# Kernel optimization log

Measured on AMD Instinct MI355X. Metric: run time of the kernel, lower is better.

The kernel has to match this reference:

```python
import jax, jax.numpy as jnp
import numpy as np

EPS = 1e-5

def _conv1x1(x, w):
    # x: (B, Cin, N, K), w: (Cout, Cin) -> (B, Cout, N, K)
    return jnp.einsum('oc,bcnk->bonk', w, x)

def _bn2d(x, gamma, beta):
    # eval-mode BN with running_mean=0, running_var=1 (fresh init)
    scale = gamma / jnp.sqrt(1.0 + EPS)
    return x * scale[None, :, None, None] + beta[None, :, None, None]

def setup_inputs() -> dict:
    key = jax.random.key(0)
    ks = jax.random.split(key, 10)
    B, Cin, N, K = 8, 64, 1024, 32
    Cout, M = 64, 8
    Cin2 = 2 * Cin  # kernel_input='w_neighbor'
    features = jax.random.normal(ks[0], (B, Cin, N, K), dtype=jnp.float32)
    points_xyz = jax.random.normal(ks[1], (B, 3, N, K), dtype=jnp.float32)
    # ScoreNet convs: mlp_channels [7,16,16,16,M]; first 3 have BN (no bias), last has bias
    w1 = jax.random.normal(ks[2], (16, 7), dtype=jnp.float32) * (2.0 / 7) ** 0.5
    w2 = jax.random.normal(ks[3], (16, 16), dtype=jnp.float32) * (2.0 / 16) ** 0.5
    w3 = jax.random.normal(ks[4], (16, 16), dtype=jnp.float32) * (2.0 / 16) ** 0.5
    w4 = jax.random.normal(ks[5], (M, 16), dtype=jnp.float32) * (2.0 / 16) ** 0.5
    b4 = jnp.zeros((M,), dtype=jnp.float32)
    g1 = jnp.ones((16,), jnp.float32); be1 = jnp.zeros((16,), jnp.float32)
    g2 = jnp.ones((16,), jnp.float32); be2 = jnp.zeros((16,), jnp.float32)
    g3 = jnp.ones((16,), jnp.float32); be3 = jnp.zeros((16,), jnp.float32)
    # weight bank: kaiming_normal on (M, 2Cin, Cout) -> stored as (2Cin, M, Cout)
    wb = jax.random.normal(ks[6], (Cin2, M, Cout), dtype=jnp.float32) * (2.0 / Cin2) ** 0.5
    bn_g = jnp.ones((Cout,), jnp.float32); bn_b = jnp.zeros((Cout,), jnp.float32)
    return dict(features=features, points_xyz=points_xyz,
                w1=w1, g1=g1, be1=be1, w2=w2, g2=g2, be2=be2,
                w3=w3, g3=g3, be3=be3, w4=w4, b4=b4,
                weight_bank=wb, bn_g=bn_g, bn_b=bn_b)

def reference(features, points_xyz, w1, g1, be1, w2, g2, be2, w3, g3, be3,
              w4, b4, weight_bank, bn_g, bn_b):
    B, Cin, N, K = features.shape
    M = weight_bank.shape[1]
    # kernel_input = 'w_neighbor': concat(feat - center, feat) -> (B, 2Cin, N, K)
    center_f = features[..., :1]
    feat = jnp.concatenate([features - center_f, features], axis=1)
    # scorenet input = 'w_neighbor_dist': (center_xyz, xyz_diff, dist) -> (B, 7, N, K)
    center_xyz = jnp.broadcast_to(points_xyz[..., :1], points_xyz.shape)
    xyz_diff = points_xyz - center_xyz
    dist = jnp.sqrt(jnp.sum(xyz_diff * xyz_diff, axis=1, keepdims=True))
    xyz_feats = jnp.concatenate([center_xyz, xyz_diff, dist], axis=1)
    h = jax.nn.relu(_bn2d(_conv1x1(xyz_feats, w1), g1, be1))
    h = jax.nn.relu(_bn2d(_conv1x1(h, w2), g2, be2))
    h = jax.nn.relu(_bn2d(_conv1x1(h, w3), g3, be3))
    s = _conv1x1(h, w4) + b4[None, :, None, None]  # (B, M, N, K)
    scores = jax.nn.softmax(s, axis=1)
    scores = jnp.transpose(scores, (0, 2, 3, 1))  # (B, N, K, M)
    # matmul with weight bank then score-weighted sum over kernels, fused via einsum
    # original: (B,N,K,2Cin)@(2Cin,M*Cout) -> (B,N,K,M,Cout); sum_m scores * . -> (B,N,K,Cout)
    new_features = jnp.einsum('bcnk,cmo,bnkm->bonk', feat, weight_bank, scores)
    # BN2d (eval, fresh stats) + ReLU
    new_features = jax.nn.relu(_bn2d(new_features, bn_g, bn_b))
    return new_features
```

## Files before the change

kernel.cpp:

```cpp
#include <hip/hip_runtime.h>
#include <hip/hip_bf16.h>

typedef _Float16 f16;
typedef __attribute__((ext_vector_type(2))) _Float16 f16x2;
typedef __attribute__((ext_vector_type(8))) _Float16 f16x8;
typedef __attribute__((ext_vector_type(16))) float f32x16;

#define BNSCL 0.9999950000375f

__global__ __launch_bounds__(256) void k_scores(
    const float* __restrict__ xyz,
    const float* __restrict__ w1, const float* __restrict__ g1, const float* __restrict__ be1,
    const float* __restrict__ w2, const float* __restrict__ g2, const float* __restrict__ be2,
    const float* __restrict__ w3, const float* __restrict__ g3, const float* __restrict__ be3,
    const float* __restrict__ w4, const float* __restrict__ b4,
    const float* __restrict__ wb, f16* __restrict__ wbtA,
    f16* __restrict__ scores)
{
    __shared__ float lw[856];
    const int tid = threadIdx.x;

    if (blockIdx.x < 256) {
        int idx = blockIdx.x * 256 + tid;
        int j    = idx & 7;
        int lane = (idx >> 3) & 63;
        int ks   = (idx >> 9) & 31;
        int bank = (idx >> 14) & 1;
        int ot   = idx >> 15;
        int c    = ks * 2 + (lane >> 5);
        int o    = ot * 32 + (lane & 31);
        float vD = wb[(c * 8 + j) * 64 + o];
        float v  = bank ? vD : vD + wb[((c + 64) * 8 + j) * 64 + o];
        wbtA[idx] = (f16)v;
    }

    if (tid < 112) lw[tid] = w1[tid];
    lw[112 + tid] = w2[tid];
    lw[368 + tid] = w3[tid];
    if (tid < 128) lw[624 + tid] = w4[tid];
    if (tid < 8)   lw[752 + tid] = b4[tid];
    if (tid < 16) {
        lw[760 + tid] = g1[tid] * BNSCL;  lw[776 + tid] = be1[tid];
        lw[792 + tid] = g2[tid] * BNSCL;  lw[808 + tid] = be2[tid];
        lw[824 + tid] = g3[tid] * BNSCL;  lw[840 + tid] = be3[tid];
    }
    __syncthreads();

    float in7[2][7], h1[2][16], h2[2][16], s[2][8];

#pragma unroll
    for (int q = 0; q < 2; ++q) {
        int g = blockIdx.x * 512 + q * 256 + tid;
        int b = g >> 15;
        int p = g & 32767;
        int pc = p & ~31;
        const float* xb = xyz + (size_t)b * 98304;
        float cx = xb[pc], cy = xb[32768 + pc], cz = xb[65536 + pc];
        float dx = xb[p] - cx, dy = xb[32768 + p] - cy, dz = xb[65536 + p] - cz;
        in7[q][0] = cx; in7[q][1] = cy; in7[q][2] = cz;
        in7[q][3] = dx; in7[q][4] = dy; in7[q][5] = dz;
        in7[q][6] = sqrtf(dx * dx + dy * dy + dz * dz);
    }

#pragma unroll
    for (int o = 0; o < 16; ++o) {
        float a0 = 0.f, a1 = 0.f;
#pragma unroll
        for (int c = 0; c < 7; ++c) {
            float w = lw[o * 7 + c];
            a0 += w * in7[0][c]; a1 += w * in7[1][c];
        }
        float gs = lw[760 + o], bb = lw[776 + o];
        h1[0][o] = fmaxf(a0 * gs + bb, 0.f);
        h1[1][o] = fmaxf(a1 * gs + bb, 0.f);
    }
#pragma unroll
    for (int o = 0; o < 16; ++o) {
        float a0 = 0.f, a1 = 0.f;
#pragma unroll
        for (int c = 0; c < 16; ++c) {
            float w = lw[112 + o * 16 + c];
            a0 += w * h1[0][c]; a1 += w * h1[1][c];
        }
        float gs = lw[792 + o], bb = lw[808 + o];
        h2[0][o] = fmaxf(a0 * gs + bb, 0.f);
        h2[1][o] = fmaxf(a1 * gs + bb, 0.f);
    }
#pragma unroll
    for (int o = 0; o < 16; ++o) {
        float a0 = 0.f, a1 = 0.f;
#pragma unroll
        for (int c = 0; c < 16; ++c) {
            float w = lw[368 + o * 16 + c];
            a0 += w * h2[0][c]; a1 += w * h2[1][c];
        }
        float gs = lw[824 + o], bb = lw[840 + o];
        h1[0][o] = fmaxf(a0 * gs + bb, 0.f);
        h1[1][o] = fmaxf(a1 * gs + bb, 0.f);
    }
#pragma unroll
    for (int o = 0; o < 8; ++o) {
        float bb = lw[752 + o];
        float a0 = bb, a1 = bb;
#pragma unroll
        for (int c = 0; c < 16; ++c) {
            float w = lw[624 + o * 16 + c];
            a0 += w * h1[0][c]; a1 += w * h1[1][c];
        }
        s[0][o] = a0; s[1][o] = a1;
    }

#pragma unroll
    for (int q = 0; q < 2; ++q) {
        int g = blockIdx.x * 512 + q * 256 + tid;
        float mx = s[q][0];
#pragma unroll
        for (int i = 1; i < 8; ++i) mx = fmaxf(mx, s[q][i]);
        float sum = 0.f;
#pragma unroll
        for (int i = 0; i < 8; ++i) { s[q][i] = __expf(s[q][i] - mx); sum += s[q][i]; }
        float inv = 1.f / sum;
        f16x8 o8;
#pragma unroll
        for (int i = 0; i < 8; ++i) o8[i] = (f16)(s[q][i] * inv);
        *(f16x8*)(scores + (size_t)g * 8) = o8;
    }
}

__global__ __launch_bounds__(1024, 4) void k_main(
    const float* __restrict__ feat,
    const f16* __restrict__ scores,
    const f16* __restrict__ wbtA,
    const float* __restrict__ bn_g, const float* __restrict__ bn_b,
    float* __restrict__ out)
{
    __shared__ __align__(16) f16 lwb[32768];
    __shared__ __align__(16) float fbuf[8][2][1024];
    __shared__ __align__(16) f16 gscr[16][512];

    const int tid  = threadIdx.x;
    const int lane = tid & 63;
    const int wave = tid >> 6;
    const int l31  = lane & 31;
    const int lh   = lane >> 5;
    const int w64  = wave * 64;

    const int ot = blockIdx.x >> 8;
    const int g  = blockIdx.x & 255;
    const int pblock = g * 1024;
    const int b    = pblock >> 15;
    const int pt0  = (pblock & 32767) + w64;
    const int pc0  = pt0 + l31;
    const int pc1  = pc0 + 32;

    const float* fb = feat + (size_t)b * 2097152;
    const float* gsrc0 = fb + (pblock & 32767) + w64 + lane;

    const f16* src = wbtA + ((size_t)ot << 15);
#pragma unroll
    for (int it = 0; it < 4; ++it) {
        int idx = it * 1024 + tid;
        *(int4*)&lwb[idx << 3] = *(const int4*)&src[idx << 3];
    }

    const int gpt = pblock + w64 + l31;
    f16x8 sv0 = *(const f16x8*)(scores + (size_t)gpt * 8);
    f16x8 sv1 = *(const f16x8*)(scores + (size_t)(gpt + 32) * 8);
    const f16x2 s0a = {sv0[0], sv0[1]}, s0b = {sv0[2], sv0[3]},
                s0c = {sv0[4], sv0[5]}, s0d = {sv0[6], sv0[7]};
    const f16x2 s1a = {sv1[0], sv1[1]}, s1b = {sv1[2], sv1[3]},
                s1c = {sv1[4], sv1[5]}, s1d = {sv1[6], sv1[7]};

    const bool mon  = (l31 < 16);
    const int  mpos = l31 & 7;
    const f16x2 mk0 = { (f16)((mon && mpos == 0) ? 1.f : 0.f),
                        (f16)((mon && mpos == 1) ? 1.f : 0.f) };
    const f16x2 mk1 = { (f16)((mon && mpos == 2) ? 1.f : 0.f),
                        (f16)((mon && mpos == 3) ? 1.f : 0.f) };
    const f16x2 mk2 = { (f16)((mon && mpos == 4) ? 1.f : 0.f),
                        (f16)((mon && mpos == 5) ? 1.f : 0.f) };
    const f16x2 mk3 = { (f16)((mon && mpos == 6) ? 1.f : 0.f),
                        (f16)((mon && mpos == 7) ? 1.f : 0.f) };

    f32x16 acc0 = {}, acc1 = {}, accG = {};
    const f16* Alds = lwb + (lane << 3);

#define STAGE(t)                                                               \
    {                                                                          \
        __builtin_amdgcn_global_load_lds(                                      \
            (const __attribute__((address_space(1))) void*)                    \
                (gsrc0 + ((size_t)(2 * (t)) << 15)),                           \
            (__attribute__((address_space(3))) void*)&fbuf[(t) & 7][0][w64],   \
            4, 0, 0);                                                          \
        __builtin_amdgcn_global_load_lds(                                      \
            (const __attribute__((address_space(1))) void*)                    \
                (gsrc0 + ((size_t)(2 * (t) + 1) << 15)),                       \
            (__attribute__((address_space(3))) void*)&fbuf[(t) & 7][1][w64],   \
            4, 0, 0);                                                          \
    }

#define WAITV(n) asm volatile("s_waitcnt vmcnt(" #n ")" ::: "memory")

    __builtin_amdgcn_sched_barrier(0);
    STAGE(0); STAGE(1); STAGE(2); STAGE(3); STAGE(4); STAGE(5);

    asm volatile("s_waitcnt lgkmcnt(0)" ::: "memory");
    __builtin_amdgcn_s_barrier();

#define KSTEP(kk)                                                              \
    {                                                                          \
        f16x8 aS = *(const f16x8*)(Alds + ((size_t)(kk) << 9));                \
        f16x8 aD = *(const f16x8*)(Alds + ((size_t)((kk) + 32) << 9));         \
        const float* frow = fbuf[(kk) & 7][lh];                                \
        float fv0 = frow[w64 + l31], fv1 = frow[w64 + l31 + 32];               \
        float fc0 = frow[w64],       fc1 = frow[w64 + 32];                     \
        float fcs = (l31 & 8) ? fc1 : fc0;                                     \
        f16 hR0 = (f16)fv0, hR1 = (f16)fv1, hC = (f16)(-fcs);                  \
        f16x2 fR0 = {hR0, hR0}, fR1 = {hR1, hR1}, fg2 = {hC, hC};              \
        f16x2 r0a = fR0 * s0a, r0b = fR0 * s0b, r0c = fR0 * s0c, r0d = fR0 * s0d; \
        f16x2 r1a = fR1 * s1a, r1b = fR1 * s1b, r1c = fR1 * s1c, r1d = fR1 * s1d; \
        f16x2 q0 = mk0 * fg2, q1 = mk1 * fg2, q2 = mk2 * fg2, q3 = mk3 * fg2;  \
        f16x8 bS0 = {r0a[0],r0a[1],r0b[0],r0b[1],r0c[0],r0c[1],r0d[0],r0d[1]}; \
        f16x8 bS1 = {r1a[0],r1a[1],r1b[0],r1b[1],r1c[0],r1c[1],r1d[0],r1d[1]}; \
        f16x8 bG  = {q0[0],q0[1],q1[0],q1[1],q2[0],q2[1],q3[0],q3[1]};         \
        acc0 = __builtin_amdgcn_mfma_f32_32x32x16_f16(aS, bS0, acc0, 0, 0, 0); \
        acc1 = __builtin_amdgcn_mfma_f32_32x32x16_f16(aS, bS1, acc1, 0, 0, 0); \
        accG = __builtin_amdgcn_mfma_f32_32x32x16_f16(aD, bG, accG, 0, 0, 0);  \
    }

#define PAIR(p)                                                                \
    STAGE(2 * (p) + 6) STAGE(2 * (p) + 7)                                      \
    WAITV(12);                                                                 \
    KSTEP(2 * (p)) KSTEP(2 * (p) + 1)

    PAIR(0)  PAIR(1)  PAIR(2)  PAIR(3)
    PAIR(4)  PAIR(5)  PAIR(6)  PAIR(7)
    PAIR(8)  PAIR(9)  PAIR(10) PAIR(11)
    PAIR(12)
    WAITV(8);
    KSTEP(26) KSTEP(27)
    WAITV(4);
    KSTEP(28) KSTEP(29)
    WAITV(0);
    KSTEP(30) KSTEP(31)
#undef PAIR
#undef KSTEP
#undef STAGE
#undef WAITV

    if (l31 < 16) {
        const int base = (l31 >> 3) * 256 + (l31 & 7);
#pragma unroll
        for (int r = 0; r < 16; ++r) {
            int o = (r & 3) + ((r >> 2) << 3) + (lh << 2);
            gscr[wave][base + o * 8] = (f16)accG[r];
        }
    }
    asm volatile("s_waitcnt lgkmcnt(0)" ::: "memory");
    __builtin_amdgcn_sched_barrier(0);
    {
        f16x8 a2 = *(const f16x8*)&gscr[wave][lh * 256 + l31 * 8];
        f16x8 z8 = {};
        f16x8 bC0 = lh ? z8 : sv0;
        f16x8 bC1 = lh ? sv1 : z8;
        acc0 = __builtin_amdgcn_mfma_f32_32x32x16_f16(a2, bC0, acc0, 0, 0, 0);
        acc1 = __builtin_amdgcn_mfma_f32_32x32x16_f16(a2, bC1, acc1, 0, 0, 0);
    }

    __builtin_amdgcn_sched_barrier(0);

#pragma unroll
    for (int r = 0; r < 16; ++r) {
        int o = ot * 32 + (r & 3) + ((r >> 2) << 3) + (lh << 2);
        float gs = bn_g[o] * BNSCL, bb = bn_b[o];
        size_t row = (size_t)(b * 64 + o) << 15;
        out[row + pc0] = fmaxf(acc0[r] * gs + bb, 0.f);
        out[row + pc1] = fmaxf(acc1[r] * gs + bb, 0.f);
    }
}

extern "C" void kernel_launch(void* const* d_in, const int* in_sizes, int n_in,
                              void* d_out, int out_size, void* d_ws, size_t ws_size,
                              hipStream_t stream)
{
    const float* features = (const float*)d_in[0];
    const float* xyz      = (const float*)d_in[1];
    const float* w1  = (const float*)d_in[2];
    const float* g1  = (const float*)d_in[3];
    const float* be1 = (const float*)d_in[4];
    const float* w2  = (const float*)d_in[5];
    const float* g2  = (const float*)d_in[6];
    const float* be2 = (const float*)d_in[7];
    const float* w3  = (const float*)d_in[8];
    const float* g3  = (const float*)d_in[9];
    const float* be3 = (const float*)d_in[10];
    const float* w4  = (const float*)d_in[11];
    const float* b4  = (const float*)d_in[12];
    const float* wb  = (const float*)d_in[13];
    const float* bn_g = (const float*)d_in[14];
    const float* bn_b = (const float*)d_in[15];

    f16* scores = (f16*)d_ws;
    f16* wbtA   = (f16*)((char*)d_ws + (4u << 20));

    k_scores<<<512, 256, 0, stream>>>(xyz, w1, g1, be1, w2, g2, be2,
                                      w3, g3, be3, w4, b4, wb, wbtA, scores);
    k_main<<<512, 1024, 0, stream>>>(features, scores, wbtA, bn_g, bn_b,
                                     (float*)d_out);
}
```

Measured before the change: 171.0 us.

## Split center-feature correction GEMM into separate kernel and halve main LDS weights

Moves the per-center correction GEMM (weight bank D half times negated center features) out of the main kernel into a new kernel that writes a small f16 matrix to workspace, which the main kernel then reads for its final MFMA. The main kernel drops one MFMA per k-step and holds only half the weight tile in LDS, which may raise occupancy. The scorenet kernel also reads its small weights straight from global memory instead of staging them in shared memory, removing a barrier. The cost is an extra launch and a second pass over the center-feature columns.

```diff
diff --git a/kernel.cpp b/kernel.cpp
--- a/kernel.cpp
+++ b/kernel.cpp
@@ -17,7 +17,6 @@
     const float* __restrict__ wb, f16* __restrict__ wbtA,
     f16* __restrict__ scores)
 {
-    __shared__ float lw[856];
     const int tid = threadIdx.x;
 
     if (blockIdx.x < 256) {
@@ -34,18 +33,6 @@
         wbtA[idx] = (f16)v;
     }
 
-    if (tid < 112) lw[tid] = w1[tid];
-    lw[112 + tid] = w2[tid];
-    lw[368 + tid] = w3[tid];
-    if (tid < 128) lw[624 + tid] = w4[tid];
-    if (tid < 8)   lw[752 + tid] = b4[tid];
-    if (tid < 16) {
-        lw[760 + tid] = g1[tid] * BNSCL;  lw[776 + tid] = be1[tid];
-        lw[792 + tid] = g2[tid] * BNSCL;  lw[808 + tid] = be2[tid];
-        lw[824 + tid] = g3[tid] * BNSCL;  lw[840 + tid] = be3[tid];
-    }
-    __syncthreads();
-
     float in7[2][7], h1[2][16], h2[2][16], s[2][8];
 
 #pragma unroll
@@ -67,10 +54,10 @@
         float a0 = 0.f, a1 = 0.f;
 #pragma unroll
         for (int c = 0; c < 7; ++c) {
-            float w = lw[o * 7 + c];
+            float w = w1[o * 7 + c];
             a0 += w * in7[0][c]; a1 += w * in7[1][c];
         }
-        float gs = lw[760 + o], bb = lw[776 + o];
+        float gs = g1[o] * BNSCL, bb = be1[o];
         h1[0][o] = fmaxf(a0 * gs + bb, 0.f);
         h1[1][o] = fmaxf(a1 * gs + bb, 0.f);
     }
@@ -79,10 +66,10 @@
         float a0 = 0.f, a1 = 0.f;
 #pragma unroll
         for (int c = 0; c < 16; ++c) {
-            float w = lw[112 + o * 16 + c];
+            float w = w2[o * 16 + c];
             a0 += w * h1[0][c]; a1 += w * h1[1][c];
         }
-        float gs = lw[792 + o], bb = lw[808 + o];
+        float gs = g2[o] * BNSCL, bb = be2[o];
         h2[0][o] = fmaxf(a0 * gs + bb, 0.f);
         h2[1][o] = fmaxf(a1 * gs + bb, 0.f);
     }
@@ -91,20 +78,20 @@
         float a0 = 0.f, a1 = 0.f;
 #pragma unroll
         for (int c = 0; c < 16; ++c) {
-            float w = lw[368 + o * 16 + c];
+            float w = w3[o * 16 + c];
             a0 += w * h2[0][c]; a1 += w * h2[1][c];
         }
-        float gs = lw[824 + o], bb = lw[840 + o];
+        float gs = g3[o] * BNSCL, bb = be3[o];
         h1[0][o] = fmaxf(a0 * gs + bb, 0.f);
         h1[1][o] = fmaxf(a1 * gs + bb, 0.f);
     }
 #pragma unroll
     for (int o = 0; o < 8; ++o) {
-        float bb = lw[752 + o];
+        float bb = b4[o];
         float a0 = bb, a1 = bb;
 #pragma unroll
         for (int c = 0; c < 16; ++c) {
-            float w = lw[624 + o * 16 + c];
+            float w = w4[o * 16 + c];
             a0 += w * h1[0][c]; a1 += w * h1[1][c];
         }
         s[0][o] = a0; s[1][o] = a1;
@@ -127,15 +114,12 @@
     }
 }
 
-__global__ __launch_bounds__(1024, 4) void k_main(
+__global__ __launch_bounds__(1024) void k_g(
     const float* __restrict__ feat,
-    const f16* __restrict__ scores,
     const f16* __restrict__ wbtA,
-    const float* __restrict__ bn_g, const float* __restrict__ bn_b,
-    float* __restrict__ out)
+    f16* __restrict__ Gt)
 {
-    __shared__ __align__(16) f16 lwb[32768];
-    __shared__ __align__(16) float fbuf[8][2][1024];
+    __shared__ __align__(16) f16 ldsD[16384];
     __shared__ __align__(16) f16 gscr[16][512];
 
     const int tid  = threadIdx.x;
@@ -143,33 +127,21 @@
     const int wave = tid >> 6;
     const int l31  = lane & 31;
     const int lh   = lane >> 5;
-    const int w64  = wave * 64;
-
-    const int ot = blockIdx.x >> 8;
-    const int g  = blockIdx.x & 255;
-    const int pblock = g * 1024;
-    const int b    = pblock >> 15;
-    const int pt0  = (pblock & 32767) + w64;
-    const int pc0  = pt0 + l31;
-    const int pc1  = pc0 + 32;
-
-    const float* fb = feat + (size_t)b * 2097152;
-    const float* gsrc0 = fb + (pblock & 32767) + w64 + lane;
-
-    const f16* src = wbtA + ((size_t)ot << 15);
-#pragma unroll
-    for (int it = 0; it < 4; ++it) {
+
+    const int ot     = blockIdx.x >> 8;
+    const int window = (blockIdx.x & 255) * 16 + wave;
+    const int ptglob = window * 64;
+    const int b      = ptglob >> 15;
+    const int ptb    = ptglob & 32767;
+    const float* fb  = feat + (size_t)b * 2097152;
+
+    const f16* src = wbtA + ot * 32768 + 16384;
+#pragma unroll
+    for (int it = 0; it < 2; ++it) {
         int idx = it * 1024 + tid;
-        *(int4*)&lwb[idx << 3] = *(const int4*)&src[idx << 3];
-    }
-
-    const int gpt = pblock + w64 + l31;
-    f16x8 sv0 = *(const f16x8*)(scores + (size_t)gpt * 8);
-    f16x8 sv1 = *(const f16x8*)(scores + (size_t)(gpt + 32) * 8);
-    const f16x2 s0a = {sv0[0], sv0[1]}, s0b = {sv0[2], sv0[3]},
-                s0c = {sv0[4], sv0[5]}, s0d = {sv0[6], sv0[7]};
-    const f16x2 s1a = {sv1[0], sv1[1]}, s1b = {sv1[2], sv1[3]},
-                s1c = {sv1[4], sv1[5]}, s1d = {sv1[6], sv1[7]};
+        *(int4*)&ldsD[idx << 3] = *(const int4*)&src[idx << 3];
+    }
+    __syncthreads();
 
     const bool mon  = (l31 < 16);
     const int  mpos = l31 & 7;
@@ -182,7 +154,83 @@
     const f16x2 mk3 = { (f16)((mon && mpos == 6) ? 1.f : 0.f),
                         (f16)((mon && mpos == 7) ? 1.f : 0.f) };
 
-    f32x16 acc0 = {}, acc1 = {}, accG = {};
+    f32x16 accG = {};
+    const f16* Ad = ldsD + (lane << 3);
+
+#pragma unroll
+    for (int kk = 0; kk < 32; ++kk) {
+        f16x8 aD = *(const f16x8*)(Ad + ((size_t)kk << 9));
+        const float* frow = fb + ((size_t)(2 * kk + lh) << 15) + ptb;
+        float fcs = (l31 & 8) ? frow[32] : frow[0];
+        f16 hC = (f16)(-fcs);
+        f16x2 fg2 = {hC, hC};
+        f16x2 q0 = mk0 * fg2, q1 = mk1 * fg2, q2 = mk2 * fg2, q3 = mk3 * fg2;
+        f16x8 bG = {q0[0],q0[1],q1[0],q1[1],q2[0],q2[1],q3[0],q3[1]};
+        accG = __builtin_amdgcn_mfma_f32_32x32x16_f16(aD, bG, accG, 0, 0, 0);
+    }
+
+    if (l31 < 16) {
+        const int base = (l31 >> 3) * 256 + (l31 & 7);
+#pragma unroll
+        for (int r = 0; r < 16; ++r) {
+            int o = (r & 3) + ((r >> 2) << 3) + (lh << 2);
+            gscr[wave][base + o * 8] = (f16)accG[r];
+        }
+    }
+    asm volatile("s_waitcnt lgkmcnt(0)" ::: "memory");
+    __builtin_amdgcn_sched_barrier(0);
+    {
+        f16x8 gv = *(const f16x8*)&gscr[wave][lh * 256 + l31 * 8];
+        size_t gg = (size_t)(window * 2 + lh);
+        *(f16x8*)&Gt[(gg * 64 + ot * 32 + l31) * 8] = gv;
+    }
+}
+
+__global__ __launch_bounds__(1024, 4) void k_main(
+    const float* __restrict__ feat,
+    const f16* __restrict__ scores,
+    const f16* __restrict__ wbtA,
+    const f16* __restrict__ Gt,
+    const float* __restrict__ bn_g, const float* __restrict__ bn_b,
+    float* __restrict__ out)
+{
+    __shared__ __align__(16) f16 lwb[16384];
+    __shared__ __align__(16) float fbuf[8][2][1024];
+
+    const int tid  = threadIdx.x;
+    const int lane = tid & 63;
+    const int wave = tid >> 6;
+    const int l31  = lane & 31;
+    const int lh   = lane >> 5;
+    const int w64  = wave * 64;
+
+    const int ot = blockIdx.x >> 8;
+    const int g  = blockIdx.x & 255;
+    const int pblock = g * 1024;
+    const int b    = pblock >> 15;
+    const int pt0  = (pblock & 32767) + w64;
+    const int pc0  = pt0 + l31;
+    const int pc1  = pc0 + 32;
+
+    const float* fb = feat + (size_t)b * 2097152;
+    const float* gsrc0 = fb + (pblock & 32767) + w64 + lane;
+
+    const f16* src = wbtA + ot * 32768;
+#pragma unroll
+    for (int it = 0; it < 2; ++it) {
+        int idx = it * 1024 + tid;
+        *(int4*)&lwb[idx << 3] = *(const int4*)&src[idx << 3];
+    }
+
+    const int gpt = pblock + w64 + l31;
+    f16x8 sv0 = *(const f16x8*)(scores + (size_t)gpt * 8);
+    f16x8 sv1 = *(const f16x8*)(scores + (size_t)(gpt + 32) * 8);
+    const f16x2 s0a = {sv0[0], sv0[1]}, s0b = {sv0[2], sv0[3]},
+                s0c = {sv0[4], sv0[5]}, s0d = {sv0[6], sv0[7]};
+    const f16x2 s1a = {sv1[0], sv1[1]}, s1b = {sv1[2], sv1[3]},
+                s1c = {sv1[4], sv1[5]}, s1d = {sv1[6], sv1[7]};
+
+    f32x16 acc0 = {}, acc1 = {};
     const f16* Alds = lwb + (lane << 3);
 
 #define STAGE(t)                                                               \
@@ -210,22 +258,16 @@
 #define KSTEP(kk)                                                              \
     {                                                                          \
         f16x8 aS = *(const f16x8*)(Alds + ((size_t)(kk) << 9));                \
-        f16x8 aD = *(const f16x8*)(Alds + ((size_t)((kk) + 32) << 9));         \
         const float* frow = fbuf[(kk) & 7][lh];                                \
         float fv0 = frow[w64 + l31], fv1 = frow[w64 + l31 + 32];               \
-        float fc0 = frow[w64],       fc1 = frow[w64 + 32];                     \
-        float fcs = (l31 & 8) ? fc1 : fc0;                                     \
-        f16 hR0 = (f16)fv0, hR1 = (f16)fv1, hC = (f16)(-fcs);                  \
-        f16x2 fR0 = {hR0, hR0}, fR1 = {hR1, hR1}, fg2 = {hC, hC};              \
+        f16 hR0 = (f16)fv0, hR1 = (f16)fv1;                                    \
+        f16x2 fR0 = {hR0, hR0}, fR1 = {hR1, hR1};                              \
         f16x2 r0a = fR0 * s0a, r0b = fR0 * s0b, r0c = fR0 * s0c, r0d = fR0 * s0d; \
         f16x2 r1a = fR1 * s1a, r1b = fR1 * s1b, r1c = fR1 * s1c, r1d = fR1 * s1d; \
-        f16x2 q0 = mk0 * fg2, q1 = mk1 * fg2, q2 = mk2 * fg2, q3 = mk3 * fg2;  \
         f16x8 bS0 = {r0a[0],r0a[1],r0b[0],r0b[1],r0c[0],r0c[1],r0d[0],r0d[1]}; \
         f16x8 bS1 = {r1a[0],r1a[1],r1b[0],r1b[1],r1c[0],r1c[1],r1d[0],r1d[1]}; \
-        f16x8 bG  = {q0[0],q0[1],q1[0],q1[1],q2[0],q2[1],q3[0],q3[1]};         \
         acc0 = __builtin_amdgcn_mfma_f32_32x32x16_f16(aS, bS0, acc0, 0, 0, 0); \
         acc1 = __builtin_amdgcn_mfma_f32_32x32x16_f16(aS, bS1, acc1, 0, 0, 0); \
-        accG = __builtin_amdgcn_mfma_f32_32x32x16_f16(aD, bG, accG, 0, 0, 0);  \
     }
 
 #define PAIR(p)                                                                \
@@ -248,26 +290,18 @@
 #undef STAGE
 #undef WAITV
 
-    if (l31 < 16) {
-        const int base = (l31 >> 3) * 256 + (l31 & 7);
-#pragma unroll
-        for (int r = 0; r < 16; ++r) {
-            int o = (r & 3) + ((r >> 2) << 3) + (lh << 2);
-            gscr[wave][base + o * 8] = (f16)accG[r];
-        }
-    }
-    asm volatile("s_waitcnt lgkmcnt(0)" ::: "memory");
     __builtin_amdgcn_sched_barrier(0);
+
     {
-        f16x8 a2 = *(const f16x8*)&gscr[wave][lh * 256 + l31 * 8];
+        const int g0 = (pblock + w64) >> 5;
+        const f16x8 a2 = *(const f16x8*)
+            &Gt[((size_t)(g0 + lh) * 64 + ot * 32 + l31) * 8];
         f16x8 z8 = {};
         f16x8 bC0 = lh ? z8 : sv0;
         f16x8 bC1 = lh ? sv1 : z8;
         acc0 = __builtin_amdgcn_mfma_f32_32x32x16_f16(a2, bC0, acc0, 0, 0, 0);
         acc1 = __builtin_amdgcn_mfma_f32_32x32x16_f16(a2, bC1, acc1, 0, 0, 0);
     }
-
-    __builtin_amdgcn_sched_barrier(0);
 
 #pragma unroll
     for (int r = 0; r < 16; ++r) {
@@ -302,9 +336,11 @@
 
     f16* scores = (f16*)d_ws;
     f16* wbtA   = (f16*)((char*)d_ws + (4u << 20));
+    f16* Gt     = (f16*)((char*)d_ws + (4u << 20) + 131072);
 
     k_scores<<<512, 256, 0, stream>>>(xyz, w1, g1, be1, w2, g2, be2,
                                       w3, g3, be3, w4, b4, wb, wbtA, scores);
-    k_main<<<512, 1024, 0, stream>>>(features, scores, wbtA, bn_g, bn_b,
-                                     (float*)d_out);
+    k_g<<<512, 1024, 0, stream>>>(features, wbtA, Gt);
+    k_main<<<512, 1024, 0, stream>>>(features, scores, wbtA, Gt,
+                                     bn_g, bn_b, (float*)d_out);
 }
```

Measured after the change: 194.4 us. 1.14x slower.
